# Performance work log

Hardware: AMD Instinct MI355X
Metric: run time of the kernel (lower is better)

Reference implementation:

```python
import jax, jax.numpy as jnp
import numpy as np

KH = KW = 3
PAD = 1
STRIDE = 1
H_OUT = W_OUT = 32  # (32 - 3 + 2)/1 + 1


def unfold2d(X):
    # torch.nn.functional.unfold ordering: feature index = c*KH*KW + i*KW + j
    B, C, H, W = X.shape
    Xp = jnp.pad(X, ((0, 0), (0, 0), (PAD, PAD), (PAD, PAD)))
    patches = [Xp[:, :, i:i + H_OUT * STRIDE:STRIDE, j:j + W_OUT * STRIDE:STRIDE]
               for i in range(KH) for j in range(KW)]
    u = jnp.stack(patches, axis=2)            # (B, C, KH*KW, H_out, W_out)
    return u.reshape(B, C * KH * KW, H_OUT * W_OUT)  # (B, K, S)


def setup_inputs() -> dict:
    key = jax.random.key(0)
    k1, k2, k3 = jax.random.split(key, 3)
    B, C_in, C_out = 64, 128, 64
    S = H_OUT * W_OUT           # 1024 spatial locations
    K = C_in * KH * KW          # 1152 unfolded features
    # xavier-uniform-ish scale for per-location weights
    lim = float(np.sqrt(6.0 / (K + C_out)))
    X = jax.random.normal(k1, (B, C_in, 32, 32), dtype=jnp.float32)
    weight = jax.random.uniform(k2, (S, K, C_out), minval=-lim, maxval=lim, dtype=jnp.float32)
    bias = jax.random.uniform(k3, (H_OUT, W_OUT), minval=-0.3, maxval=0.3, dtype=jnp.float32)
    return {"X": X, "weight": weight, "bias": bias}


def reference(X, weight, bias):
    B = X.shape[0]
    C_out = weight.shape[-1]
    ufld = unfold2d(X)                          # (B, K, S)
    ufld = ufld + bias.reshape(1, 1, -1)        # per-location bias added to unfolded values
    h = jnp.einsum('bks,skc->bcs', ufld, weight)  # per-location batched GEMM
    return h.reshape(B, C_out, H_OUT, W_OUT)
```

## Files before the change

### kernel.cpp

```cpp
#include <hip/hip_runtime.h>

typedef short v8s __attribute__((ext_vector_type(8)));
typedef float v4f __attribute__((ext_vector_type(4)));

__device__ __forceinline__ unsigned rne_hi(float f) {
    unsigned u = __float_as_uint(f);
    return u + 0x7FFFu + ((u >> 16) & 1u);
}

#if defined(__has_builtin)
#if __has_builtin(__builtin_amdgcn_cvt_pk_bf16_f32)
#define HAVE_PK_BF16 1
#endif
#endif

__device__ __forceinline__ unsigned pk_bf16(float lo, float hi) {
#ifdef HAVE_PK_BF16
    auto r = __builtin_amdgcn_cvt_pk_bf16_f32(lo, hi);
    unsigned u;
    __builtin_memcpy(&u, &r, 4);
    return u;
#else
    return (rne_hi(lo) >> 16) | (rne_hi(hi) & 0xFFFF0000u);
#endif
}

__device__ __forceinline__ void barrier_raw() {
    asm volatile("s_barrier" ::: "memory");
}
__device__ __forceinline__ void barrier_lgkm() {
    asm volatile("s_waitcnt lgkmcnt(0)\n\ts_barrier" ::: "memory");
}

__global__ __launch_bounds__(256) void xpose_kernel(const float* __restrict__ X,
                                                    unsigned short* __restrict__ Xt) {
    __shared__ float tile[64][65];
    const int bx  = blockIdx.x;
    const int c   = bx >> 4;
    const int hw0 = (bx & 15) << 6;
    const int t    = threadIdx.x;
    const int lane = t & 63;
    const int brow = t >> 6;

    if (bx == 0 && t < 128) Xt[8388608 + t] = 0;

#pragma unroll
    for (int r = 0; r < 16; ++r) {
        int b = brow + (r << 2);
        tile[b][lane] = __builtin_nontemporal_load(
            &X[((size_t)(b * 128 + c) << 10) + hw0 + lane]);
    }
    __syncthreads();
#pragma unroll
    for (int r = 0; r < 16; ++r) {
        int row = brow + (r << 2);
        float f = tile[lane][row];
        Xt[((((size_t)c << 10) + hw0 + row) << 6) + lane] =
            (unsigned short)(rne_hi(f) >> 16);
    }
}

__global__ __launch_bounds__(256, 4) void vconv_kernel(
    const float* __restrict__ Wg,
    const float* __restrict__ bias,
    const unsigned short* __restrict__ Xt,
    unsigned short* __restrict__ scratch)
{
    __shared__ __align__(16) unsigned A_lds[2][1024];
    __shared__ __align__(16) unsigned B_lds[2][1024];
    __shared__ int tab[1152];
    __shared__ float csum[16][65];
    __shared__ float csum_tot[64];

    const int s = blockIdx.x;
    const int y = s >> 5, x = s & 31;
    const int t    = threadIdx.x;
    const int lane = t & 63;
    const int wv   = t >> 6;
    const int mh   = wv >> 1, nh = wv & 1;

    for (int k = t; k < 1152; k += 256) {
        int c  = k / 9;
        int r  = k - c * 9;
        int di = r / 3, dj = r - di * 3;
        int yy = y + di - 1, xx = x + dj - 1;
        int off = ((c << 10) + (yy << 5) + xx) << 7;
        bool ok = (yy >= 0) && (yy < 32) && (xx >= 0) && (xx < 32);
        tab[k] = ok ? off : 16777216;
    }

    const float bias_s = bias[s];

    const int g16 = t & 15;
    const int hi4 = t >> 4;
    const int r4  = g16 << 2;

    const float* wbase = Wg + ((size_t)s * 1152 + (hi4 << 1)) * 64 + r4;
    const char*  xb    = (const char*)Xt + (r4 << 1);

    unsigned waddr[4];
#pragma unroll
    for (int i = 0; i < 4; ++i) {
        int row = r4 + i;
        unsigned grp = (unsigned)((hi4 >> 2) ^ ((row >> 2) & 3));
        waddr[i] = (unsigned)(row << 4) + (grp << 2) + (unsigned)(hi4 & 3);
    }

    const int quad = lane >> 4, l15 = lane & 15;
    unsigned a_raddr[2], b_raddr[2];
#pragma unroll
    for (int i = 0; i < 2; ++i) {
        int ra = (((mh << 1) + i) << 4) + l15;
        a_raddr[i] = (unsigned)(ra << 4) + ((unsigned)(quad ^ ((ra >> 2) & 3)) << 2);
        int rb = (((nh << 1) + i) << 4) + l15;
        b_raddr[i] = (unsigned)(rb << 4) + ((unsigned)(quad ^ ((rb >> 2) & 3)) << 2);
    }

    v4f acc[2][2];
#pragma unroll
    for (int i = 0; i < 2; ++i)
#pragma unroll
        for (int j = 0; j < 2; ++j) acc[i][j] = (v4f){0.f, 0.f, 0.f, 0.f};
    float cs0 = 0.f, cs1 = 0.f, cs2 = 0.f, cs3 = 0.f;

    barrier_lgkm();

    v4f Fa0, Fb0, Fa1, Fb1;
    uint2  P0, Q0, P1, Q1;

    auto LOAD = [&](int kk2) {
        const v4f* wb = (const v4f*)(wbase + (size_t)kk2 * 4096);
        Fa0 = __builtin_nontemporal_load(wb);
        Fb0 = __builtin_nontemporal_load(wb + 16);
        Fa1 = __builtin_nontemporal_load(wb + 512);
        Fb1 = __builtin_nontemporal_load(wb + 528);
        int kb  = (kk2 << 6) + (hi4 << 1);
        int o00 = tab[kb], o01 = tab[kb + 1];
        int o10 = tab[kb + 32], o11 = tab[kb + 33];
        P0 = *(const uint2*)(xb + o00);
        Q0 = *(const uint2*)(xb + o01);
        P1 = *(const uint2*)(xb + o10);
        Q1 = *(const uint2*)(xb + o11);
    };

    LOAD(0);

    for (int kk = 0; kk < 18; ++kk) {
        barrier_raw();

        B_lds[0][waddr[0]] = pk_bf16(Fa0.x, Fb0.x);
        B_lds[0][waddr[1]] = pk_bf16(Fa0.y, Fb0.y);
        B_lds[0][waddr[2]] = pk_bf16(Fa0.z, Fb0.z);
        B_lds[0][waddr[3]] = pk_bf16(Fa0.w, Fb0.w);
        A_lds[0][waddr[0]] = __builtin_amdgcn_perm(Q0.x, P0.x, 0x05040100u);
        A_lds[0][waddr[1]] = __builtin_amdgcn_perm(Q0.x, P0.x, 0x07060302u);
        A_lds[0][waddr[2]] = __builtin_amdgcn_perm(Q0.y, P0.y, 0x05040100u);
        A_lds[0][waddr[3]] = __builtin_amdgcn_perm(Q0.y, P0.y, 0x07060302u);
        B_lds[1][waddr[0]] = pk_bf16(Fa1.x, Fb1.x);
        B_lds[1][waddr[1]] = pk_bf16(Fa1.y, Fb1.y);
        B_lds[1][waddr[2]] = pk_bf16(Fa1.z, Fb1.z);
        B_lds[1][waddr[3]] = pk_bf16(Fa1.w, Fb1.w);
        A_lds[1][waddr[0]] = __builtin_amdgcn_perm(Q1.x, P1.x, 0x05040100u);
        A_lds[1][waddr[1]] = __builtin_amdgcn_perm(Q1.x, P1.x, 0x07060302u);
        A_lds[1][waddr[2]] = __builtin_amdgcn_perm(Q1.y, P1.y, 0x05040100u);
        A_lds[1][waddr[3]] = __builtin_amdgcn_perm(Q1.y, P1.y, 0x07060302u);

        cs0 += (Fa0.x + Fb0.x) + (Fa1.x + Fb1.x);
        cs1 += (Fa0.y + Fb0.y) + (Fa1.y + Fb1.y);
        cs2 += (Fa0.z + Fb0.z) + (Fa1.z + Fb1.z);
        cs3 += (Fa0.w + Fb0.w) + (Fa1.w + Fb1.w);

        if (kk < 17) LOAD(kk + 1);

        barrier_lgkm();

#pragma unroll
        for (int h = 0; h < 2; ++h) {
            v8s a0 = *(const v8s*)&A_lds[h][a_raddr[0]];
            v8s a1 = *(const v8s*)&A_lds[h][a_raddr[1]];
            v8s b0 = *(const v8s*)&B_lds[h][b_raddr[0]];
            v8s b1 = *(const v8s*)&B_lds[h][b_raddr[1]];
            acc[0][0] = __builtin_amdgcn_mfma_f32_16x16x32_bf16(a0, b0, acc[0][0], 0, 0, 0);
            acc[0][1] = __builtin_amdgcn_mfma_f32_16x16x32_bf16(a0, b1, acc[0][1], 0, 0, 0);
            acc[1][0] = __builtin_amdgcn_mfma_f32_16x16x32_bf16(a1, b0, acc[1][0], 0, 0, 0);
            acc[1][1] = __builtin_amdgcn_mfma_f32_16x16x32_bf16(a1, b1, acc[1][1], 0, 0, 0);
        }
    }

    csum[hi4][r4 + 0] = cs0;
    csum[hi4][r4 + 1] = cs1;
    csum[hi4][r4 + 2] = cs2;
    csum[hi4][r4 + 3] = cs3;
    barrier_lgkm();
    if (t < 64) {
        float tot = 0.f;
#pragma unroll
        for (int p = 0; p < 16; ++p) tot += csum[p][t];
        csum_tot[t] = tot;
    }
    barrier_lgkm();

    unsigned short* sb = scratch + ((size_t)s << 12);
#pragma unroll
    for (int j = 0; j < 2; ++j) {
        int n = (((nh << 1) + j) << 4) + l15;
        float cb = bias_s * csum_tot[n];
#pragma unroll
        for (int i = 0; i < 2; ++i) {
#pragma unroll
            for (int r = 0; r < 4; ++r) {
                int m = (((mh << 1) + i) << 4) + (quad << 2) + r;
                sb[(m << 6) + n] = (unsigned short)(rne_hi(acc[i][j][r] + cb) >> 16);
            }
        }
    }
}

__global__ __launch_bounds__(256) void otrans_kernel(const unsigned short* __restrict__ S,
                                                     float* __restrict__ out) {
    __shared__ unsigned short tile[64][66];
    const int bx = blockIdx.x;
    const int m0 = (bx & 63) << 6;
    const int s0 = (bx >> 6) << 6;
    const int t = threadIdx.x, lane = t & 63, brow = t >> 6;
#pragma unroll
    for (int r = 0; r < 16; ++r) {
        int row = brow + (r << 2);
        tile[row][lane] = S[((size_t)(s0 + row) << 12) + m0 + lane];
    }
    __syncthreads();
#pragma unroll
    for (int r = 0; r < 16; ++r) {
        int row = brow + (r << 2);
        float f = __uint_as_float((unsigned)tile[lane][row] << 16);
        __builtin_nontemporal_store(f, &out[((size_t)(m0 + row) << 10) + s0 + lane]);
    }
}

extern "C" void kernel_launch(void* const* d_in, const int* in_sizes, int n_in,
                              void* d_out, int out_size, void* d_ws, size_t ws_size,
                              hipStream_t stream) {
    const float* X    = (const float*)d_in[0];
    const float* Wg   = (const float*)d_in[1];
    const float* bias = (const float*)d_in[2];
    float* out = (float*)d_out;

    unsigned short* Xt = (unsigned short*)d_ws;
    unsigned short* scratch = (unsigned short*)((char*)d_ws + 16777472);

    xpose_kernel<<<2048, 256, 0, stream>>>(X, Xt);
    vconv_kernel<<<1024, 256, 0, stream>>>(Wg, bias, Xt, scratch);
    otrans_kernel<<<1024, 256, 0, stream>>>(scratch, out);
}
```

Before: 414.6 us.

## Double-buffer LDS tiles and prefetch weights two stages ahead

Splits the A/B LDS tiles into two ping-pong buffers and unrolls the K loop by two, which drops the leading barrier in each iteration. Weight loads are now issued two steps ahead and im2col activation loads one step ahead, so more global traffic is in flight while MFMAs run. The csum reduction scratch is aliased onto the now-idle A buffer to offset the extra LDS. The cost is higher register and LDS pressure, which could hurt occupancy at four blocks per CU.

```diff
diff --git a/kernel.cpp b/kernel.cpp
--- a/kernel.cpp
+++ b/kernel.cpp
@@ -25,9 +25,6 @@
 #endif
 }
 
-__device__ __forceinline__ void barrier_raw() {
-    asm volatile("s_barrier" ::: "memory");
-}
 __device__ __forceinline__ void barrier_lgkm() {
     asm volatile("s_waitcnt lgkmcnt(0)\n\ts_barrier" ::: "memory");
 }
@@ -60,17 +57,79 @@
     }
 }
 
+
+#define LOADA_SET(KK, P0d, Q0d, P1d, Q1d) do {                                  \
+    int kb_ = ((KK) << 6) + (hi4 << 1);                                         \
+    int o00_ = tab[kb_], o01_ = tab[kb_ + 1];                                   \
+    int o10_ = tab[kb_ + 32], o11_ = tab[kb_ + 33];                             \
+    P0d = *(const uint2*)(xb + o00_);                                           \
+    Q0d = *(const uint2*)(xb + o01_);                                           \
+    P1d = *(const uint2*)(xb + o10_);                                           \
+    Q1d = *(const uint2*)(xb + o11_);                                           \
+} while (0)
+
+#define LOADW_SET(KK, FA0d, FB0d, FA1d, FB1d) do {                              \
+    const v4f* wb_ = (const v4f*)(wbase + (size_t)(KK) * 4096);                 \
+    FA0d = __builtin_nontemporal_load(wb_);                                     \
+    FB0d = __builtin_nontemporal_load(wb_ + 16);                                \
+    FA1d = __builtin_nontemporal_load(wb_ + 512);                               \
+    FB1d = __builtin_nontemporal_load(wb_ + 528);                               \
+} while (0)
+
+#define MFMA_H(BUF, H) do {                                                     \
+    const unsigned* Ah_ = &A_lds[BUF][H][0];                                    \
+    const unsigned* Bh_ = &B_lds[BUF][H][0];                                    \
+    v8s a0_ = *(const v8s*)&Ah_[a_raddr[0]];                                    \
+    v8s a1_ = *(const v8s*)&Ah_[a_raddr[1]];                                    \
+    v8s b0_ = *(const v8s*)&Bh_[b_raddr[0]];                                    \
+    v8s b1_ = *(const v8s*)&Bh_[b_raddr[1]];                                    \
+    acc[0][0] = __builtin_amdgcn_mfma_f32_16x16x32_bf16(a0_, b0_, acc[0][0], 0, 0, 0); \
+    acc[0][1] = __builtin_amdgcn_mfma_f32_16x16x32_bf16(a0_, b1_, acc[0][1], 0, 0, 0); \
+    acc[1][0] = __builtin_amdgcn_mfma_f32_16x16x32_bf16(a1_, b0_, acc[1][0], 0, 0, 0); \
+    acc[1][1] = __builtin_amdgcn_mfma_f32_16x16x32_bf16(a1_, b1_, acc[1][1], 0, 0, 0); \
+} while (0)
+
+#define VBODY(KK, BUF, P0, Q0, P1, Q1, P0n, Q0n, P1n, Q1n, FA0, FB0, FA1, FB1) do { \
+    if ((KK) < 17) { LOADA_SET((KK) + 1, P0n, Q0n, P1n, Q1n); }                 \
+    {                                                                           \
+        unsigned* Ab_ = &A_lds[BUF][0][0];                                      \
+        unsigned* Bb_ = &B_lds[BUF][0][0];                                      \
+        Bb_[waddr[0]] = pk_bf16(FA0.x, FB0.x);                                  \
+        Bb_[waddr[1]] = pk_bf16(FA0.y, FB0.y);                                  \
+        Bb_[waddr[2]] = pk_bf16(FA0.z, FB0.z);                                  \
+        Bb_[waddr[3]] = pk_bf16(FA0.w, FB0.w);                                  \
+        Bb_[1024 + waddr[0]] = pk_bf16(FA1.x, FB1.x);                           \
+        Bb_[1024 + waddr[1]] = pk_bf16(FA1.y, FB1.y);                           \
+        Bb_[1024 + waddr[2]] = pk_bf16(FA1.z, FB1.z);                           \
+        Bb_[1024 + waddr[3]] = pk_bf16(FA1.w, FB1.w);                           \
+        Ab_[waddr[0]] = __builtin_amdgcn_perm(Q0.x, P0.x, 0x05040100u);         \
+        Ab_[waddr[1]] = __builtin_amdgcn_perm(Q0.x, P0.x, 0x07060302u);         \
+        Ab_[waddr[2]] = __builtin_amdgcn_perm(Q0.y, P0.y, 0x05040100u);         \
+        Ab_[waddr[3]] = __builtin_amdgcn_perm(Q0.y, P0.y, 0x07060302u);         \
+        Ab_[1024 + waddr[0]] = __builtin_amdgcn_perm(Q1.x, P1.x, 0x05040100u);  \
+        Ab_[1024 + waddr[1]] = __builtin_amdgcn_perm(Q1.x, P1.x, 0x07060302u);  \
+        Ab_[1024 + waddr[2]] = __builtin_amdgcn_perm(Q1.y, P1.y, 0x05040100u);  \
+        Ab_[1024 + waddr[3]] = __builtin_amdgcn_perm(Q1.y, P1.y, 0x07060302u);  \
+        cs0 += (FA0.x + FB0.x) + (FA1.x + FB1.x);                               \
+        cs1 += (FA0.y + FB0.y) + (FA1.y + FB1.y);                               \
+        cs2 += (FA0.z + FB0.z) + (FA1.z + FB1.z);                               \
+        cs3 += (FA0.w + FB0.w) + (FA1.w + FB1.w);                               \
+        if ((KK) < 16) { LOADW_SET((KK) + 2, FA0, FB0, FA1, FB1); }             \
+    }                                                                           \
+    barrier_lgkm();                                                             \
+    MFMA_H(BUF, 0);                                                             \
+    MFMA_H(BUF, 1);                                                             \
+} while (0)
+
 __global__ __launch_bounds__(256, 4) void vconv_kernel(
     const float* __restrict__ Wg,
     const float* __restrict__ bias,
     const unsigned short* __restrict__ Xt,
     unsigned short* __restrict__ scratch)
 {
-    __shared__ __align__(16) unsigned A_lds[2][1024];
-    __shared__ __align__(16) unsigned B_lds[2][1024];
+    __shared__ __align__(16) unsigned A_lds[2][2][1024];
+    __shared__ __align__(16) unsigned B_lds[2][2][1024];
     __shared__ int tab[1152];
-    __shared__ float csum[16][65];
-    __shared__ float csum_tot[64];
 
     const int s = blockIdx.x;
     const int y = s >> 5, x = s & 31;
@@ -125,68 +184,20 @@
 
     barrier_lgkm();
 
-    v4f Fa0, Fb0, Fa1, Fb1;
-    uint2  P0, Q0, P1, Q1;
-
-    auto LOAD = [&](int kk2) {
-        const v4f* wb = (const v4f*)(wbase + (size_t)kk2 * 4096);
-        Fa0 = __builtin_nontemporal_load(wb);
-        Fb0 = __builtin_nontemporal_load(wb + 16);
-        Fa1 = __builtin_nontemporal_load(wb + 512);
-        Fb1 = __builtin_nontemporal_load(wb + 528);
-        int kb  = (kk2 << 6) + (hi4 << 1);
-        int o00 = tab[kb], o01 = tab[kb + 1];
-        int o10 = tab[kb + 32], o11 = tab[kb + 33];
-        P0 = *(const uint2*)(xb + o00);
-        Q0 = *(const uint2*)(xb + o01);
-        P1 = *(const uint2*)(xb + o10);
-        Q1 = *(const uint2*)(xb + o11);
-    };
-
-    LOAD(0);
-
-    for (int kk = 0; kk < 18; ++kk) {
-        barrier_raw();
-
-        B_lds[0][waddr[0]] = pk_bf16(Fa0.x, Fb0.x);
-        B_lds[0][waddr[1]] = pk_bf16(Fa0.y, Fb0.y);
-        B_lds[0][waddr[2]] = pk_bf16(Fa0.z, Fb0.z);
-        B_lds[0][waddr[3]] = pk_bf16(Fa0.w, Fb0.w);
-        A_lds[0][waddr[0]] = __builtin_amdgcn_perm(Q0.x, P0.x, 0x05040100u);
-        A_lds[0][waddr[1]] = __builtin_amdgcn_perm(Q0.x, P0.x, 0x07060302u);
-        A_lds[0][waddr[2]] = __builtin_amdgcn_perm(Q0.y, P0.y, 0x05040100u);
-        A_lds[0][waddr[3]] = __builtin_amdgcn_perm(Q0.y, P0.y, 0x07060302u);
-        B_lds[1][waddr[0]] = pk_bf16(Fa1.x, Fb1.x);
-        B_lds[1][waddr[1]] = pk_bf16(Fa1.y, Fb1.y);
-        B_lds[1][waddr[2]] = pk_bf16(Fa1.z, Fb1.z);
-        B_lds[1][waddr[3]] = pk_bf16(Fa1.w, Fb1.w);
-        A_lds[1][waddr[0]] = __builtin_amdgcn_perm(Q1.x, P1.x, 0x05040100u);
-        A_lds[1][waddr[1]] = __builtin_amdgcn_perm(Q1.x, P1.x, 0x07060302u);
-        A_lds[1][waddr[2]] = __builtin_amdgcn_perm(Q1.y, P1.y, 0x05040100u);
-        A_lds[1][waddr[3]] = __builtin_amdgcn_perm(Q1.y, P1.y, 0x07060302u);
-
-        cs0 += (Fa0.x + Fb0.x) + (Fa1.x + Fb1.x);
-        cs1 += (Fa0.y + Fb0.y) + (Fa1.y + Fb1.y);
-        cs2 += (Fa0.z + Fb0.z) + (Fa1.z + Fb1.z);
-        cs3 += (Fa0.w + Fb0.w) + (Fa1.w + Fb1.w);
-
-        if (kk < 17) LOAD(kk + 1);
-
-        barrier_lgkm();
-
-#pragma unroll
-        for (int h = 0; h < 2; ++h) {
-            v8s a0 = *(const v8s*)&A_lds[h][a_raddr[0]];
-            v8s a1 = *(const v8s*)&A_lds[h][a_raddr[1]];
-            v8s b0 = *(const v8s*)&B_lds[h][b_raddr[0]];
-            v8s b1 = *(const v8s*)&B_lds[h][b_raddr[1]];
-            acc[0][0] = __builtin_amdgcn_mfma_f32_16x16x32_bf16(a0, b0, acc[0][0], 0, 0, 0);
-            acc[0][1] = __builtin_amdgcn_mfma_f32_16x16x32_bf16(a0, b1, acc[0][1], 0, 0, 0);
-            acc[1][0] = __builtin_amdgcn_mfma_f32_16x16x32_bf16(a1, b0, acc[1][0], 0, 0, 0);
-            acc[1][1] = __builtin_amdgcn_mfma_f32_16x16x32_bf16(a1, b1, acc[1][1], 0, 0, 0);
-        }
-    }
-
+    uint2 P0a, Q0a, P1a, Q1a, P0b, Q0b, P1b, Q1b;
+    v4f FA0a, FB0a, FA1a, FB1a, FA0b, FB0b, FA1b, FB1b;
+
+    LOADA_SET(0, P0a, Q0a, P1a, Q1a);
+    LOADW_SET(0, FA0a, FB0a, FA1a, FB1a);
+    LOADW_SET(1, FA0b, FB0b, FA1b, FB1b);
+
+    for (int kk = 0; kk < 18; kk += 2) {
+        VBODY(kk,     0, P0a, Q0a, P1a, Q1a, P0b, Q0b, P1b, Q1b, FA0a, FB0a, FA1a, FB1a);
+        VBODY(kk + 1, 1, P0b, Q0b, P1b, Q1b, P0a, Q0a, P1a, Q1a, FA0b, FB0b, FA1b, FB1b);
+    }
+
+    float (*csum)[65]  = (float (*)[65]) & A_lds[0][0][0];
+    float* csum_tot    = ((float*)&A_lds[0][0][0]) + 16 * 65;
     csum[hi4][r4 + 0] = cs0;
     csum[hi4][r4 + 1] = cs1;
     csum[hi4][r4 + 2] = cs2;
```

Result: no change. 415.3 us (+0.2%).
